# Kernel optimization log

Hardware: AMD Instinct MI355X
Metric: run time of the kernel (lower is better)

Reference implementation:

```python
import jax, jax.numpy as jnp
import numpy as np

EPS = 1e-7  # dummy-column epsilon from stanza utils.add_dummy(eps=True)


def setup_inputs() -> dict:
    key = jax.random.key(0)
    ks = jax.random.split(key, 9)
    n_mentions, emb = 10000, 1024
    batch, n_ants, pw_emb = 1024, 64, 64
    hidden = 1024
    in_features = 3 * emb + pw_emb  # 3136
    return {
        "all_mentions": jax.random.normal(ks[0], (n_mentions, emb), jnp.float32),
        "mentions_batch": jax.random.normal(ks[1], (batch, emb), jnp.float32),
        "pw_batch": jax.random.normal(ks[2], (batch, n_ants, pw_emb), jnp.float32),
        "top_indices_batch": jax.random.randint(ks[3], (batch, n_ants), 0, n_mentions),
        "top_rough_scores_batch": jax.random.normal(ks[4], (batch, n_ants), jnp.float32),
        "W1": jax.random.normal(ks[5], (hidden, in_features), jnp.float32) * 0.02,
        "b1": jax.random.normal(ks[6], (hidden,), jnp.float32) * 0.02,
        "Wout": jax.random.normal(ks[7], (1, hidden), jnp.float32) * 0.02,
        "bout": jax.random.normal(ks[8], (1,), jnp.float32) * 0.02,
    }


def reference(all_mentions, mentions_batch, pw_batch, top_indices_batch,
              top_rough_scores_batch, W1, b1, Wout, bout):
    n_ants = pw_batch.shape[1]
    # pair matrix: [batch, n_ants, 3*emb + pw_emb]
    a = jnp.broadcast_to(mentions_batch[:, None, :],
                         (mentions_batch.shape[0], n_ants, mentions_batch.shape[1]))
    b = all_mentions[top_indices_batch]          # gather: [batch, n_ants, emb]
    pair = jnp.concatenate((a, b, a * b, pw_batch), axis=2)
    # FFNN: Linear -> LeakyReLU (dropout is identity at eval) -> Linear(->1)
    h = jax.nn.leaky_relu(jnp.einsum('bnf,hf->bnh', pair, W1) + b1, negative_slope=0.01)
    ffnn = (jnp.einsum('bnh,oh->bno', h, Wout) + bout)[..., 0]  # [batch, n_ants]
    scores = top_rough_scores_batch + ffnn
    # add dummy column with eps at position 0 -> [batch, n_ants + 1]
    dummy = jnp.full((scores.shape[0], 1), EPS, scores.dtype)
    return jnp.concatenate((dummy, scores), axis=1)
```

## Files before the change

### kernel.cpp

```cpp
#include <hip/hip_runtime.h>
#include <hip/hip_bf16.h>
#include <cstdint>
#include <cstdio>

typedef unsigned short u16;
typedef unsigned int   u32;
typedef __attribute__((ext_vector_type(8))) short bf16x8;
typedef __attribute__((ext_vector_type(4))) float f32x4;
typedef __attribute__((ext_vector_type(4))) u16   u16x4;

#define GLOBAL_AS __attribute__((address_space(1)))
#define LDS_AS    __attribute__((address_space(3)))

static __device__ __forceinline__ u16 f2bf(float f) {
  u32 u = __builtin_bit_cast(u32, f);
  u = (u + 0x7fffu + ((u >> 16) & 1u)) >> 16;
  return (u16)u;
}
static __device__ __forceinline__ float bf2f(u16 v) {
  return __builtin_bit_cast(float, (u32)v << 16);
}
static __device__ __forceinline__ void gload_lds16(const void* g, void* l) {
  __builtin_amdgcn_global_load_lds((GLOBAL_AS u32*)g, (LDS_AS u32*)l, 16, 0, 0);
}

__global__ void k_cvt(const float* __restrict__ src, int ld, int c0,
                      int rows_src, int cols4, int total4,
                      u16* __restrict__ dst, int ldd, int dcol) {
  int gid = blockIdx.x * 256 + threadIdx.x;
  if (gid >= total4) return;
  int r = gid / cols4;
  int c = (gid - r * cols4) * 4;
  u16x4 o = {0, 0, 0, 0};
  if (r < rows_src) {
    const float4 v = *(const float4*)&src[(size_t)r * ld + c0 + c];
    o[0] = f2bf(v.x); o[1] = f2bf(v.y); o[2] = f2bf(v.z); o[3] = f2bf(v.w);
  }
  *(u16x4*)&dst[(size_t)r * ldd + dcol + c] = o;
}

__global__ void k_init(const float* __restrict__ rough,
                       const float* __restrict__ bout,
                       float* __restrict__ out) {
  int i = blockIdx.x * 256 + threadIdx.x;
  if (i >= 1024 * 65) return;
  int bi = i / 65, c = i - bi * 65;
  out[i] = (c == 0) ? 1e-7f : rough[bi * 64 + c - 1] + bout[0];
}

__global__ void k_build_cmat(const float* __restrict__ ments,
                             const float* __restrict__ allm,
                             const float* __restrict__ pw,
                             const int* __restrict__ topidx,
                             u16* __restrict__ Cmat, int r0) {
  int gid = blockIdx.x * 256 + threadIdx.x;
  int lr = gid / 272;
  int c4 = gid - lr * 272;
  int r  = r0 + lr;
  int bi = r >> 6;
  u16x4 o;
  if (c4 < 256) {
    int k   = c4 * 4;
    int idx = topidx[r];
    float4 a = *(const float4*)&ments[(size_t)bi * 1024 + k];
    float4 b = *(const float4*)&allm[(size_t)idx * 1024 + k];
    o[0] = f2bf(a.x * b.x); o[1] = f2bf(a.y * b.y);
    o[2] = f2bf(a.z * b.z); o[3] = f2bf(a.w * b.w);
  } else {
    int k = (c4 - 256) * 4;
    float4 p = *(const float4*)&pw[(size_t)r * 64 + k];
    o[0] = f2bf(p.x); o[1] = f2bf(p.y); o[2] = f2bf(p.z); o[3] = f2bf(p.w);
  }
  *(u16x4*)&Cmat[(size_t)lr * 1088 + c4 * 4] = o;
}

__global__ __launch_bounds__(256)
void gemm128(const u16* __restrict__ A, int lda,
             const u16* __restrict__ B, int ldb, int Ksteps,
             u16* __restrict__ C, int ldc) {
  __shared__ u16 As[128 * 64];
  __shared__ u16 Bs[128 * 64];
  const int t = threadIdx.x;
  const int w = t >> 6, l = t & 63;
  const int wr = w >> 1, wc = w & 1;
  const int brow = blockIdx.x * 128;
  const int bcol = blockIdx.y * 128;
  const int srow = t >> 3;
  const int scol = (t & 7) * 8;
  const int gsw  = (((t & 7) ^ ((t >> 3) & 7))) * 8;

  f32x4 acc[4][4] = {};
  for (int ks = 0; ks < Ksteps; ++ks) {
    const int kb = ks * 64;
#pragma unroll
    for (int q = 0; q < 4; ++q) {
      int r = q * 32 + srow;
      gload_lds16(A + (size_t)(brow + r) * lda + kb + gsw, &As[r * 64 + scol]);
      gload_lds16(B + (size_t)(bcol + r) * ldb + kb + gsw, &Bs[r * 64 + scol]);
    }
    __syncthreads();
#pragma unroll
    for (int kk = 0; kk < 2; ++kk) {
      bf16x8 af[4], bfr[4];
      const int pg = ((kk * 4 + (l >> 4)) ^ (l & 7)) * 8;
#pragma unroll
      for (int m = 0; m < 4; ++m)
        af[m] = *(const bf16x8*)&As[(wr * 64 + m * 16 + (l & 15)) * 64 + pg];
#pragma unroll
      for (int n = 0; n < 4; ++n)
        bfr[n] = *(const bf16x8*)&Bs[(wc * 64 + n * 16 + (l & 15)) * 64 + pg];
#pragma unroll
      for (int m = 0; m < 4; ++m)
#pragma unroll
        for (int n = 0; n < 4; ++n)
          acc[m][n] = __builtin_amdgcn_mfma_f32_16x16x32_bf16(af[m], bfr[n], acc[m][n], 0, 0, 0);
    }
    __syncthreads();
  }
#pragma unroll
  for (int m = 0; m < 4; ++m)
#pragma unroll
    for (int n = 0; n < 4; ++n)
#pragma unroll
      for (int reg = 0; reg < 4; ++reg) {
        int row = brow + wr * 64 + m * 16 + (l >> 4) * 4 + reg;
        int col = bcol + wc * 64 + n * 16 + (l & 15);
        C[(size_t)row * ldc + col] = f2bf(acc[m][n][reg]);
      }
}

template<bool FUSED>
__global__ __launch_bounds__(512, 1)
void gemm256(const u16* __restrict__ A, int lda,
             const u16* __restrict__ B, int ldb, int NT,
             u16* __restrict__ C, int ldc,
             const u16* __restrict__ Aproj, const u16* __restrict__ Bproj,
             const float* __restrict__ b1, const float* __restrict__ Wout,
             const int* __restrict__ topidx, float* __restrict__ out, int r0) {
  extern __shared__ u16 lds[];
  u16* As = lds;
  u16* Bs = lds + 2 * 2 * 128 * 64;

  const int t = threadIdx.x;
  const int l = t & 63;
  const int w = t >> 6;
  const int wrow = w >> 2, wcol = w & 3;
  const int brow = blockIdx.x * 256;
  const int bcol = blockIdx.y * 256;

  const int sr  = t >> 3;
  const int sc  = (t & 7) * 8;
  const int gsw = ((t & 7) ^ (sr & 7)) * 8;

  auto stageTile = [&](int kt) {
    const int cb = kt & 1;
#pragma unroll
    for (int s = 0; s < 4; ++s) {
      int lr = sr + 64 * s;
      gload_lds16(B + (size_t)(bcol + lr) * ldb + kt * 64 + gsw,
                  &Bs[(cb * 256 + lr) * 64 + sc]);
    }
#pragma unroll
    for (int h = 0; h < 2; ++h)
#pragma unroll
      for (int s = 0; s < 2; ++s) {
        int lr = sr + 64 * s;
        int g  = ((lr >> 5) << 6) + h * 32 + (lr & 31);
        gload_lds16(A + (size_t)(brow + g) * lda + kt * 64 + gsw,
                    &As[((cb * 2 + h) * 128 + lr) * 64 + sc]);
      }
  };

  f32x4 acc[8][4] = {};

  stageTile(0);
  asm volatile("s_waitcnt vmcnt(2)" ::: "memory");
  __builtin_amdgcn_s_barrier();

  for (int kt = 0; kt < NT; ++kt) {
    const int cbuf = kt & 1;
    const bool have_next = (kt + 1 < NT);
    bf16x8 bfr[4][2];
#pragma unroll
    for (int q = 0; q < 4; ++q) {
      if (q == 0) {
#pragma unroll
        for (int n = 0; n < 4; ++n) {
          int row = wcol * 64 + n * 16 + (l & 15);
#pragma unroll
          for (int kk = 0; kk < 2; ++kk) {
            int gran = (kk * 4 + (l >> 4)) ^ (l & 7);
            bfr[n][kk] = *(const bf16x8*)&Bs[(cbuf * 256 + row) * 64 + gran * 8];
          }
        }
      }
      bf16x8 af[2][2];
#pragma unroll
      for (int m2 = 0; m2 < 2; ++m2) {
        int m = 2 * q + m2;
        int g = wrow * 128 + m * 16 + (l & 15);
        int lra = ((g >> 6) << 5) + (g & 31);
#pragma unroll
        for (int kk = 0; kk < 2; ++kk) {
          int gran = (kk * 4 + (l >> 4)) ^ (l & 7);
          af[m2][kk] = *(const bf16x8*)&As[((cbuf * 2 + (q & 1)) * 128 + lra) * 64 + gran * 8];
        }
      }

      if (q == 0 && have_next) stageTile(kt + 1);

      __builtin_amdgcn_s_barrier();
      asm volatile("s_waitcnt lgkmcnt(0)" ::: "memory");
      __builtin_amdgcn_sched_barrier(0);
      __builtin_amdgcn_s_setprio(1);
#pragma unroll
      for (int m2 = 0; m2 < 2; ++m2)
#pragma unroll
        for (int n = 0; n < 4; ++n)
#pragma unroll
          for (int kk = 0; kk < 2; ++kk)
            acc[2 * q + m2][n] = __builtin_amdgcn_mfma_f32_16x16x32_bf16(
                af[m2][kk], bfr[n][kk], acc[2 * q + m2][n], 0, 0, 0);
      __builtin_amdgcn_s_setprio(0);

      if (q == 0) {
        if (have_next) asm volatile("s_waitcnt vmcnt(8)" ::: "memory");
        else           asm volatile("s_waitcnt vmcnt(0)" ::: "memory");
      } else if (q == 3 && have_next) {
        asm volatile("s_waitcnt vmcnt(2)" ::: "memory");
      }
      __builtin_amdgcn_s_barrier();
    }
  }

  if constexpr (FUSED) {
    float b1c[4], wo[4];
#pragma unroll
    for (int n = 0; n < 4; ++n) {
      int col = bcol + wcol * 64 + n * 16 + (l & 15);
      b1c[n] = b1[col];
      wo[n]  = Wout[col];
    }
#pragma unroll
    for (int m = 0; m < 8; ++m) {
#pragma unroll
      for (int reg = 0; reg < 4; ++reg) {
        int gr = r0 + brow + wrow * 128 + m * 16 + (l >> 4) * 4 + reg;
        int bi = gr >> 6;
        int mi = topidx[gr];
        float s = 0.f;
#pragma unroll
        for (int n = 0; n < 4; ++n) {
          int col = bcol + wcol * 64 + n * 16 + (l & 15);
          float v = acc[m][n][reg] + bf2f(Aproj[(size_t)bi * 1024 + col])
                  + bf2f(Bproj[(size_t)mi * 1024 + col]) + b1c[n];
          v = v > 0.f ? v : 0.01f * v;
          s += v * wo[n];
        }
        s += __shfl_xor(s, 1);
        s += __shfl_xor(s, 2);
        s += __shfl_xor(s, 4);
        s += __shfl_xor(s, 8);
        if ((l & 15) == 0)
          atomicAdd(&out[bi * 65 + 1 + (gr & 63)], s);
      }
    }
  } else {
#pragma unroll
    for (int m = 0; m < 8; ++m)
#pragma unroll
      for (int n = 0; n < 4; ++n)
#pragma unroll
        for (int reg = 0; reg < 4; ++reg) {
          int row = brow + wrow * 128 + m * 16 + (l >> 4) * 4 + reg;
          int col = bcol + wcol * 64 + n * 16 + (l & 15);
          C[(size_t)row * ldc + col] = f2bf(acc[m][n][reg]);
        }
  }
}

extern "C" void kernel_launch(void* const* d_in, const int* in_sizes, int n_in,
                              void* d_out, int out_size, void* d_ws, size_t ws_size,
                              hipStream_t stream) {
  const float* allm  = (const float*)d_in[0];
  const float* ments = (const float*)d_in[1];
  const float* pw    = (const float*)d_in[2];
  const int*   tidx  = (const int*)d_in[3];
  const float* rough = (const float*)d_in[4];
  const float* W1    = (const float*)d_in[5];
  const float* b1    = (const float*)d_in[6];
  const float* Wout  = (const float*)d_in[7];
  const float* bout  = (const float*)d_in[8];
  float* out = (float*)d_out;

  const int CHUNK = 16384;
  u16* A16    = (u16*)d_ws;
  u16* allm16 = A16 + 1024 * 1024;
  u16* W1a    = allm16 + 10240 * 1024;
  u16* W1b    = W1a + 1024 * 1024;
  u16* W1cp   = W1b + 1024 * 1024;
  u16* Aproj  = W1cp + 1024 * 1088;
  u16* Bproj  = Aproj + 1024 * 1024;
  u16* Cmat   = Bproj + 10240 * 1024;

  size_t need = (size_t)2 * ((size_t)1024*1024 + 10240*1024 + 1024*1024 + 1024*1024
              + 1024*1088 + 1024*1024 + 10240*1024 + (size_t)CHUNK*1088);
  if (ws_size < need) {
    fprintf(stderr, "kernel_launch: ws_size %zu < needed %zu\n", ws_size, need);
    return;
  }

  hipFuncSetAttribute((const void*)&gemm256<false>,
                      hipFuncAttributeMaxDynamicSharedMemorySize, 131072);
  hipFuncSetAttribute((const void*)&gemm256<true>,
                      hipFuncAttributeMaxDynamicSharedMemorySize, 131072);

  {
    int t4;
    t4 = 1024 * 256;
    k_cvt<<<(t4 + 255) / 256, 256, 0, stream>>>(W1, 3136, 0,    1024, 256, t4, W1a, 1024, 0);
    k_cvt<<<(t4 + 255) / 256, 256, 0, stream>>>(W1, 3136, 1024, 1024, 256, t4, W1b, 1024, 0);
    k_cvt<<<(t4 + 255) / 256, 256, 0, stream>>>(W1, 3136, 2048, 1024, 256, t4, W1cp, 1088, 0);
    t4 = 1024 * 16;
    k_cvt<<<(t4 + 255) / 256, 256, 0, stream>>>(W1, 3136, 3072, 1024, 16, t4, W1cp, 1088, 1024);
    t4 = 1024 * 256;
    k_cvt<<<(t4 + 255) / 256, 256, 0, stream>>>(ments, 1024, 0, 1024, 256, t4, A16, 1024, 0);
    t4 = 10240 * 256;
    k_cvt<<<(t4 + 255) / 256, 256, 0, stream>>>(allm, 1024, 0, 10000, 256, t4, allm16, 1024, 0);
  }

  gemm128<<<dim3(8, 8), 256, 0, stream>>>(A16, 1024, W1a, 1024, 16, Aproj, 1024);
  gemm256<false><<<dim3(40, 4), 512, 131072, stream>>>(allm16, 1024, W1b, 1024, 16,
                                                       Bproj, 1024,
                                                       nullptr, nullptr, nullptr, nullptr,
                                                       nullptr, nullptr, 0);

  k_init<<<260, 256, 0, stream>>>(rough, bout, out);

  for (int c = 0; c < 4; ++c) {
    int r0 = c * CHUNK;
    k_build_cmat<<<(CHUNK * 272) / 256, 256, 0, stream>>>(ments, allm, pw, tidx, Cmat, r0);
    gemm256<true><<<dim3(CHUNK / 256, 4), 512, 131072, stream>>>(Cmat, 1088, W1cp, 1088, 17,
                                                                 nullptr, 0,
                                                                 Aproj, Bproj, b1, Wout,
                                                                 tidx, out, r0);
  }
}
```

Measured before the change: 394.6 us.

## Split GEMM staging into per-quarter A/B loads, stage Bproj via LDS, fold bias

The main GEMM now issues its global-to-LDS loads in four pieces, one per MFMA quarter. A tiles are prefetched one step ahead and B tiles two steps ahead, with adjusted vmcnt waits, to spread memory traffic across the inner loop. The fused epilogue gathers the Bproj rows into LDS with async loads and caches the Aproj values per thread, replacing scattered per-element global reads. The b1 bias is folded into the Aproj GEMM, and the pair-product build reads the bf16 copies with 8-wide vectors. The a*b input is now formed from bf16-rounded operands, which slightly changes numerics.

After: 319.9 us, median of 2. -18.9%, faster.

```diff
diff --git a/kernel.cpp b/kernel.cpp
--- a/kernel.cpp
+++ b/kernel.cpp
@@ -8,6 +8,7 @@
 typedef __attribute__((ext_vector_type(8))) short bf16x8;
 typedef __attribute__((ext_vector_type(4))) float f32x4;
 typedef __attribute__((ext_vector_type(4))) u16   u16x4;
+typedef __attribute__((ext_vector_type(8))) u16   u16x8;
 
 #define GLOBAL_AS __attribute__((address_space(1)))
 #define LDS_AS    __attribute__((address_space(3)))
@@ -48,36 +49,38 @@
   out[i] = (c == 0) ? 1e-7f : rough[bi * 64 + c - 1] + bout[0];
 }
 
-__global__ void k_build_cmat(const float* __restrict__ ments,
-                             const float* __restrict__ allm,
+__global__ void k_build_cmat(const u16* __restrict__ A16,
+                             const u16* __restrict__ allm16,
                              const float* __restrict__ pw,
                              const int* __restrict__ topidx,
                              u16* __restrict__ Cmat, int r0) {
   int gid = blockIdx.x * 256 + threadIdx.x;
-  int lr = gid / 272;
-  int c4 = gid - lr * 272;
+  int lr = gid / 136;
+  int c8 = gid - lr * 136;
   int r  = r0 + lr;
-  int bi = r >> 6;
-  u16x4 o;
-  if (c4 < 256) {
-    int k   = c4 * 4;
+  u16x8 o;
+  if (c8 < 128) {
+    int k   = c8 * 8;
     int idx = topidx[r];
-    float4 a = *(const float4*)&ments[(size_t)bi * 1024 + k];
-    float4 b = *(const float4*)&allm[(size_t)idx * 1024 + k];
-    o[0] = f2bf(a.x * b.x); o[1] = f2bf(a.y * b.y);
-    o[2] = f2bf(a.z * b.z); o[3] = f2bf(a.w * b.w);
+    int bi  = r >> 6;
+    u16x8 a = *(const u16x8*)&A16[(size_t)bi * 1024 + k];
+    u16x8 b = *(const u16x8*)&allm16[(size_t)idx * 1024 + k];
+#pragma unroll
+    for (int j = 0; j < 8; ++j) o[j] = f2bf(bf2f(a[j]) * bf2f(b[j]));
   } else {
-    int k = (c4 - 256) * 4;
-    float4 p = *(const float4*)&pw[(size_t)r * 64 + k];
-    o[0] = f2bf(p.x); o[1] = f2bf(p.y); o[2] = f2bf(p.z); o[3] = f2bf(p.w);
-  }
-  *(u16x4*)&Cmat[(size_t)lr * 1088 + c4 * 4] = o;
+    int k = (c8 - 128) * 8;
+    float4 p0 = *(const float4*)&pw[(size_t)r * 64 + k];
+    float4 p1 = *(const float4*)&pw[(size_t)r * 64 + k + 4];
+    o[0] = f2bf(p0.x); o[1] = f2bf(p0.y); o[2] = f2bf(p0.z); o[3] = f2bf(p0.w);
+    o[4] = f2bf(p1.x); o[5] = f2bf(p1.y); o[6] = f2bf(p1.z); o[7] = f2bf(p1.w);
+  }
+  *(u16x8*)&Cmat[(size_t)lr * 1088 + c8 * 8] = o;
 }
 
 __global__ __launch_bounds__(256)
 void gemm128(const u16* __restrict__ A, int lda,
              const u16* __restrict__ B, int ldb, int Ksteps,
-             u16* __restrict__ C, int ldc) {
+             u16* __restrict__ C, int ldc, const float* __restrict__ bias) {
   __shared__ u16 As[128 * 64];
   __shared__ u16 Bs[128 * 64];
   const int t = threadIdx.x;
@@ -125,7 +128,8 @@
       for (int reg = 0; reg < 4; ++reg) {
         int row = brow + wr * 64 + m * 16 + (l >> 4) * 4 + reg;
         int col = bcol + wc * 64 + n * 16 + (l & 15);
-        C[(size_t)row * ldc + col] = f2bf(acc[m][n][reg]);
+        float v = acc[m][n][reg] + (bias ? bias[col] : 0.f);
+        C[(size_t)row * ldc + col] = f2bf(v);
       }
 }
 
@@ -135,7 +139,7 @@
              const u16* __restrict__ B, int ldb, int NT,
              u16* __restrict__ C, int ldc,
              const u16* __restrict__ Aproj, const u16* __restrict__ Bproj,
-             const float* __restrict__ b1, const float* __restrict__ Wout,
+             const float* __restrict__ Wout,
              const int* __restrict__ topidx, float* __restrict__ out, int r0) {
   extern __shared__ u16 lds[];
   u16* As = lds;
@@ -152,34 +156,35 @@
   const int sc  = (t & 7) * 8;
   const int gsw = ((t & 7) ^ (sr & 7)) * 8;
 
-  auto stageTile = [&](int kt) {
-    const int cb = kt & 1;
-#pragma unroll
-    for (int s = 0; s < 4; ++s) {
+  auto stageA = [&](int kt, int h) {
+    if (kt >= NT) return;
+#pragma unroll
+    for (int s = 0; s < 2; ++s) {
       int lr = sr + 64 * s;
+      int g  = ((lr >> 5) << 6) + h * 32 + (lr & 31);
+      gload_lds16(A + (size_t)(brow + g) * lda + kt * 64 + gsw,
+                  &As[(((kt & 1) * 2 + h) * 128 + lr) * 64 + sc]);
+    }
+  };
+  auto stageB = [&](int kt, int h) {
+    if (kt >= NT) return;
+#pragma unroll
+    for (int s = 0; s < 2; ++s) {
+      int lr = h * 128 + sr + 64 * s;
       gload_lds16(B + (size_t)(bcol + lr) * ldb + kt * 64 + gsw,
-                  &Bs[(cb * 256 + lr) * 64 + sc]);
-    }
-#pragma unroll
-    for (int h = 0; h < 2; ++h)
-#pragma unroll
-      for (int s = 0; s < 2; ++s) {
-        int lr = sr + 64 * s;
-        int g  = ((lr >> 5) << 6) + h * 32 + (lr & 31);
-        gload_lds16(A + (size_t)(brow + g) * lda + kt * 64 + gsw,
-                    &As[((cb * 2 + h) * 128 + lr) * 64 + sc]);
-      }
+                  &Bs[((kt & 1) * 256 + lr) * 64 + sc]);
+    }
   };
 
   f32x4 acc[8][4] = {};
 
-  stageTile(0);
-  asm volatile("s_waitcnt vmcnt(2)" ::: "memory");
+  stageB(0, 0); stageB(0, 1); stageA(0, 0); stageA(0, 1);
+  stageB(1, 0); stageB(1, 1);
+  asm volatile("s_waitcnt vmcnt(6)" ::: "memory");
   __builtin_amdgcn_s_barrier();
 
   for (int kt = 0; kt < NT; ++kt) {
     const int cbuf = kt & 1;
-    const bool have_next = (kt + 1 < NT);
     bf16x8 bfr[4][2];
 #pragma unroll
     for (int q = 0; q < 4; ++q) {
@@ -207,8 +212,12 @@
         }
       }
 
-      if (q == 0 && have_next) stageTile(kt + 1);
-
+      if      (q == 0) stageA(kt + 1, 0);
+      else if (q == 1) stageA(kt + 1, 1);
+      else if (q == 2) stageB(kt + 2, 0);
+      else             stageB(kt + 2, 1);
+
+      if (q == 0) asm volatile("s_waitcnt lgkmcnt(8)" ::: "memory");
       __builtin_amdgcn_s_barrier();
       asm volatile("s_waitcnt lgkmcnt(0)" ::: "memory");
       __builtin_amdgcn_sched_barrier(0);
@@ -224,36 +233,50 @@
       __builtin_amdgcn_s_setprio(0);
 
       if (q == 0) {
-        if (have_next) asm volatile("s_waitcnt vmcnt(8)" ::: "memory");
-        else           asm volatile("s_waitcnt vmcnt(0)" ::: "memory");
-      } else if (q == 3 && have_next) {
-        asm volatile("s_waitcnt vmcnt(2)" ::: "memory");
+        if (kt + 1 < NT) asm volatile("s_waitcnt vmcnt(6)" ::: "memory");
+        else             asm volatile("s_waitcnt vmcnt(0)" ::: "memory");
+      } else if (q == 3 && kt + 1 < NT) {
+        if (kt + 2 < NT) asm volatile("s_waitcnt vmcnt(6)" ::: "memory");
+        else             asm volatile("s_waitcnt vmcnt(2)" ::: "memory");
       }
       __builtin_amdgcn_s_barrier();
     }
   }
 
   if constexpr (FUSED) {
-    float b1c[4], wo[4];
+    __syncthreads();
+    u16* Pb = lds;
+#pragma unroll
+    for (int pass = 0; pass < 16; ++pass) {
+      int rr = pass * 16 + (t >> 5);
+      int mi = topidx[r0 + brow + rr];
+      int cc = (t & 31) * 8;
+      gload_lds16(&Bproj[(size_t)mi * 1024 + bcol + cc], &Pb[rr * 256 + cc]);
+    }
+    asm volatile("s_waitcnt vmcnt(0)" ::: "memory");
+    __syncthreads();
+
+    float wo[4], av[2][4];
+    const int bi0 = ((r0 + brow) >> 6) + wrow * 2;
 #pragma unroll
     for (int n = 0; n < 4; ++n) {
       int col = bcol + wcol * 64 + n * 16 + (l & 15);
-      b1c[n] = b1[col];
-      wo[n]  = Wout[col];
+      wo[n] = Wout[col];
+#pragma unroll
+      for (int j = 0; j < 2; ++j)
+        av[j][n] = bf2f(Aproj[(size_t)(bi0 + j) * 1024 + col]);
     }
 #pragma unroll
     for (int m = 0; m < 8; ++m) {
 #pragma unroll
       for (int reg = 0; reg < 4; ++reg) {
-        int gr = r0 + brow + wrow * 128 + m * 16 + (l >> 4) * 4 + reg;
-        int bi = gr >> 6;
-        int mi = topidx[gr];
+        int lrow = wrow * 128 + m * 16 + (l >> 4) * 4 + reg;
+        int gr = r0 + brow + lrow;
         float s = 0.f;
 #pragma unroll
         for (int n = 0; n < 4; ++n) {
-          int col = bcol + wcol * 64 + n * 16 + (l & 15);
-          float v = acc[m][n][reg] + bf2f(Aproj[(size_t)bi * 1024 + col])
-                  + bf2f(Bproj[(size_t)mi * 1024 + col]) + b1c[n];
+          int lcol = wcol * 64 + n * 16 + (l & 15);
+          float v = acc[m][n][reg] + av[m >> 2][n] + bf2f(Pb[lrow * 256 + lcol]);
           v = v > 0.f ? v : 0.01f * v;
           s += v * wo[n];
         }
@@ -262,7 +285,7 @@
         s += __shfl_xor(s, 4);
         s += __shfl_xor(s, 8);
         if ((l & 15) == 0)
-          atomicAdd(&out[bi * 65 + 1 + (gr & 63)], s);
+          atomicAdd(&out[(gr >> 6) * 65 + 1 + (gr & 63)], s);
       }
     }
   } else {
@@ -329,20 +352,20 @@
     k_cvt<<<(t4 + 255) / 256, 256, 0, stream>>>(allm, 1024, 0, 10000, 256, t4, allm16, 1024, 0);
   }
 
-  gemm128<<<dim3(8, 8), 256, 0, stream>>>(A16, 1024, W1a, 1024, 16, Aproj, 1024);
+  gemm128<<<dim3(8, 8), 256, 0, stream>>>(A16, 1024, W1a, 1024, 16, Aproj, 1024, b1);
   gemm256<false><<<dim3(40, 4), 512, 131072, stream>>>(allm16, 1024, W1b, 1024, 16,
                                                        Bproj, 1024,
-                                                       nullptr, nullptr, nullptr, nullptr,
+                                                       nullptr, nullptr, nullptr,
                                                        nullptr, nullptr, 0);
 
   k_init<<<260, 256, 0, stream>>>(rough, bout, out);
 
   for (int c = 0; c < 4; ++c) {
     int r0 = c * CHUNK;
-    k_build_cmat<<<(CHUNK * 272) / 256, 256, 0, stream>>>(ments, allm, pw, tidx, Cmat, r0);
+    k_build_cmat<<<(CHUNK * 136) / 256, 256, 0, stream>>>(A16, allm16, pw, tidx, Cmat, r0);
     gemm256<true><<<dim3(CHUNK / 256, 4), 512, 131072, stream>>>(Cmat, 1088, W1cp, 1088, 17,
                                                                  nullptr, 0,
-                                                                 Aproj, Bproj, b1, Wout,
+                                                                 Aproj, Bproj, Wout,
                                                                  tidx, out, r0);
   }
 }
```
